# Performance work log

Hardware: AMD Instinct MI355X
Metric: run time of the kernel (lower is better)

The kernel has to match this reference:

```python
import jax, jax.numpy as jnp
import numpy as np

N_NODES = 100000
N_EDGES = 3200000
HIDDEN = 64
OUT = 30


def _graph_conv(x, src, dst, W, b, n_nodes):
    # DGL GraphConv with norm='both': D_out^{-1/2} -> aggregate -> D_in^{-1/2} -> W -> +b
    ones = jnp.ones(src.shape[0], dtype=x.dtype)
    deg_out = jax.ops.segment_sum(ones, src, num_segments=n_nodes)
    deg_in = jax.ops.segment_sum(ones, dst, num_segments=n_nodes)
    norm_out = jnp.where(deg_out > 0, jax.lax.rsqrt(jnp.maximum(deg_out, 1e-30)), 0.0)
    norm_in = jnp.where(deg_in > 0, jax.lax.rsqrt(jnp.maximum(deg_in, 1e-30)), 0.0)
    h = x * norm_out[:, None]                    # [N, F] scaled source features
    msg = h[src]                                 # [E, F] gather
    agg = jax.ops.segment_sum(msg, dst, num_segments=n_nodes)  # [N, F] scatter-add
    agg = agg * norm_in[:, None]
    return agg @ W + b


def setup_inputs() -> dict:
    key = jax.random.key(0)
    k1, k2, k3, k4, k5 = jax.random.split(key, 5)
    x = jax.random.normal(k1, (N_NODES, HIDDEN), dtype=jnp.float32)
    src = jax.random.randint(k2, (N_EDGES,), 0, N_NODES, dtype=jnp.int32)
    dst = jax.random.randint(k3, (N_EDGES,), 0, N_NODES, dtype=jnp.int32)
    W1 = jax.random.normal(k4, (HIDDEN, HIDDEN), dtype=jnp.float32) / np.sqrt(HIDDEN)
    b1 = jnp.zeros((HIDDEN,), dtype=jnp.float32)
    W2 = jax.random.normal(k5, (HIDDEN, OUT), dtype=jnp.float32) / np.sqrt(HIDDEN)
    b2 = jnp.zeros((OUT,), dtype=jnp.float32)
    return {"x": x, "src": src, "dst": dst, "W1": W1, "b1": b1, "W2": W2, "b2": b2}


def reference(x, src, dst, W1, b1, W2, b2):
    h = _graph_conv(x, src, dst, W1, b1, N_NODES)
    h = jax.nn.relu(h)                           # conv1 activation=F.relu
    out = _graph_conv(h, src, dst, W2, b2, N_NODES)  # conv2: no activation
    return out
```

## Files before the change

kernel.cpp:

```cpp
#include <hip/hip_runtime.h>


#define NN 100000
#define NE 3200000
#define NOUTF 30
#define TPB 256
#define TPBW 1024
#define TPBS 512

#define DSH 8
#define DCB 256
#define DNB ((NN + DCB - 1) / DCB)
#define SSH 10
#define SCB 1024
#define SNB ((NN + SCB - 1) / SCB)

#define CHUNK 8192
#define NBLK ((NE + CHUNK - 1) / CHUNK)
#define HLD (DNB * NBLK)
#define HLS (SNB * NBLK)
#define HLT (HLD + HLS)
#define EPT (CHUNK / TPBS)

#define GCH 1024
#define NSC ((HLT + GCH - 1) / GCH)

#define POOL 9216

__device__ __forceinline__ unsigned short f2bf(float f) {
  unsigned u = __float_as_uint(f);
  u = (u + 0x7FFFu + ((u >> 16) & 1u)) >> 16;
  return (unsigned short)u;
}

__device__ __forceinline__ void acc8(float* a, const uint4& u) {
  a[0] += __uint_as_float(u.x << 16);
  a[1] += __uint_as_float(u.x & 0xFFFF0000u);
  a[2] += __uint_as_float(u.y << 16);
  a[3] += __uint_as_float(u.y & 0xFFFF0000u);
  a[4] += __uint_as_float(u.z << 16);
  a[5] += __uint_as_float(u.z & 0xFFFF0000u);
  a[6] += __uint_as_float(u.w << 16);
  a[7] += __uint_as_float(u.w & 0xFFFF0000u);
}

__device__ __forceinline__ int xcd_swz(int orig, int n) {
  int q = n / 8, r = n % 8;
  int xcd = orig % 8, idx = orig / 8;
  return (xcd < r ? xcd * (q + 1) : r * (q + 1) + (xcd - r) * q) + idx;
}

__global__ __launch_bounds__(TPBW) void k_hist(const int* __restrict__ src,
                                               const int* __restrict__ dst,
                                               int* __restrict__ H) {
  __shared__ int hd[DNB], hs[SNB];
  int t = threadIdx.x, k = blockIdx.x;
  for (int b = t; b < DNB; b += TPBW) hd[b] = 0;
  for (int b = t; b < SNB; b += TPBW) hs[b] = 0;
  __syncthreads();
  int beg = k * CHUNK, end = min(NE, beg + CHUNK);
  for (int i = beg + t; i < end; i += TPBW) {
    atomicAdd(&hd[dst[i] >> DSH], 1);
    atomicAdd(&hs[src[i] >> SSH], 1);
  }
  __syncthreads();
  for (int b = t; b < DNB; b += TPBW) H[b * NBLK + k] = hd[b];
  for (int b = t; b < SNB; b += TPBW) H[HLD + b * NBLK + k] = hs[b];
}

__global__ __launch_bounds__(TPB) void g_scan1(const int* __restrict__ a,
                                               int* __restrict__ bsums) {
  int t = threadIdx.x;
  int base = blockIdx.x * GCH + t * 4;
  int s = 0;
#pragma unroll
  for (int j = 0; j < 4; ++j) { int idx = base + j; if (idx < HLT) s += a[idx]; }
  __shared__ int red[TPB];
  red[t] = s; __syncthreads();
  for (int off = TPB / 2; off > 0; off >>= 1) {
    if (t < off) red[t] += red[t + off];
    __syncthreads();
  }
  if (t == 0) bsums[blockIdx.x] = red[0];
}

__global__ __launch_bounds__(1024) void g_scan2(int* __restrict__ bsums) {
  int t = threadIdx.x;
  __shared__ int lds[1024];
  int v = (t < NSC) ? bsums[t] : 0;
  int acc = v; lds[t] = acc; __syncthreads();
  for (int off = 1; off < 1024; off <<= 1) {
    int add = (t >= off) ? lds[t - off] : 0; __syncthreads();
    acc += add; lds[t] = acc; __syncthreads();
  }
  if (t < NSC) bsums[t] = acc - v;
}

__global__ __launch_bounds__(TPB) void g_scan3(int* __restrict__ a,
                                               const int* __restrict__ bsums) {
  int t = threadIdx.x;
  int base = blockIdx.x * GCH + t * 4;
  int v[4]; int s = 0;
#pragma unroll
  for (int j = 0; j < 4; ++j) {
    int idx = base + j;
    v[j] = (idx < HLT) ? a[idx] : 0;
    s += v[j];
  }
  __shared__ int lds[TPB];
  int acc = s; lds[t] = acc; __syncthreads();
  for (int off = 1; off < TPB; off <<= 1) {
    int add = (t >= off) ? lds[t - off] : 0; __syncthreads();
    acc += add; lds[t] = acc; __syncthreads();
  }
  int run = bsums[blockIdx.x] + (acc - s);
#pragma unroll
  for (int j = 0; j < 4; ++j) {
    int idx = base + j;
    if (idx < HLT) a[idx] = run;
    run += v[j];
  }
}

__global__ __launch_bounds__(TPBS) void k_scatter(const int* __restrict__ src,
                                                  const int* __restrict__ dst,
                                                  const int* __restrict__ Hsc,
                                                  int* __restrict__ packed,
                                                  unsigned short* __restrict__ ss) {
  __shared__ int pack_lds[CHUNK];
  __shared__ unsigned short ss_lds[CHUNK];
  __shared__ int baseD[DNB + 1], curD[DNB];
  __shared__ int baseS[SNB + 1], curS[SNB];
  __shared__ int scanbuf[TPBS];
  int t = threadIdx.x;
  int k = xcd_swz((int)blockIdx.x, NBLK);
  int beg = k * CHUNK, end = min(NE, beg + CHUNK);
  int cnt = end - beg;

  int es[EPT], ed[EPT];
#pragma unroll
  for (int j = 0; j < EPT; ++j) {
    int i = beg + j * TPBS + t;
    if (i < end) { es[j] = src[i]; ed[j] = dst[i]; }
    else { es[j] = -1; ed[j] = -1; }
  }

  for (int b = t; b < DNB; b += TPBS) curD[b] = 0;
  for (int b = t; b < SNB; b += TPBS) curS[b] = 0;
  __syncthreads();
#pragma unroll
  for (int j = 0; j < EPT; ++j) {
    if (ed[j] >= 0) {
      atomicAdd(&curD[ed[j] >> DSH], 1);
      atomicAdd(&curS[es[j] >> SSH], 1);
    }
  }
  __syncthreads();

  {
    int v = (t < DNB) ? curD[t] : 0;
    int acc = v; scanbuf[t] = acc; __syncthreads();
    for (int off = 1; off < TPBS; off <<= 1) {
      int add = (t >= off) ? scanbuf[t - off] : 0; __syncthreads();
      acc += add; scanbuf[t] = acc; __syncthreads();
    }
    if (t < DNB) baseD[t] = acc - v;
    if (t == 0) baseD[DNB] = cnt;
  }
  __syncthreads();
  {
    int v = (t < SNB) ? curS[t] : 0;
    int acc = v; scanbuf[t] = acc; __syncthreads();
    for (int off = 1; off < TPBS; off <<= 1) {
      int add = (t >= off) ? scanbuf[t - off] : 0; __syncthreads();
      acc += add; scanbuf[t] = acc; __syncthreads();
    }
    if (t < SNB) baseS[t] = acc - v;
    if (t == 0) baseS[SNB] = cnt;
  }
  __syncthreads();
  for (int b = t; b < DNB; b += TPBS) curD[b] = baseD[b];
  for (int b = t; b < SNB; b += TPBS) curS[b] = baseS[b];
  __syncthreads();

#pragma unroll
  for (int j = 0; j < EPT; ++j) {
    if (ed[j] >= 0) {
      int p = atomicAdd(&curD[ed[j] >> DSH], 1);
      pack_lds[p] = (es[j] << DSH) | (ed[j] & (DCB - 1));
      int q = atomicAdd(&curS[es[j] >> SSH], 1);
      ss_lds[q] = (unsigned short)(es[j] & (SCB - 1));
    }
  }
  __syncthreads();

  for (int i = t; i < cnt; i += TPBS) {
    int lo = 0, hi = DNB;
    while (hi - lo > 1) { int mid = (lo + hi) >> 1; if (baseD[mid] <= i) lo = mid; else hi = mid; }
    packed[Hsc[lo * NBLK + k] + (i - baseD[lo])] = pack_lds[i];
  }
  for (int i = t; i < cnt; i += TPBS) {
    int lo = 0, hi = SNB;
    while (hi - lo > 1) { int mid = (lo + hi) >> 1; if (baseS[mid] <= i) lo = mid; else hi = mid; }
    ss[Hsc[HLD + lo * NBLK + k] + (i - baseS[lo]) - NE] = ss_lds[i];
  }
}

__global__ __launch_bounds__(TPB) void k_fine_sort(const int* __restrict__ Hsc,
                                                   const int* __restrict__ packed,
                                                   int* __restrict__ src_sorted,
                                                   int* __restrict__ row_ptr,
                                                   float* __restrict__ norm_in) {
  __shared__ int hist[DCB], scn[DCB], cur[DCB];
  __shared__ int pool[POOL];
  int t = threadIdx.x, b = blockIdx.x;
  int seg_beg = Hsc[b * NBLK];
  int seg_end = (b + 1 < DNB) ? Hsc[(b + 1) * NBLK] : NE;
  int cnt = seg_end - seg_beg;
  hist[t] = 0;
  __syncthreads();
  for (int i = seg_beg + t; i < seg_end; i += TPB)
    atomicAdd(&hist[packed[i] & (DCB - 1)], 1);
  __syncthreads();
  scn[t] = hist[t];
  __syncthreads();
  for (int off = 1; off < DCB; off <<= 1) {
    int add = (t >= off) ? scn[t - off] : 0;
    __syncthreads();
    scn[t] += add;
    __syncthreads();
  }
  {
    int excl = scn[t] - hist[t];
    cur[t] = excl;
    int node = b * DCB + t;
    if (node < NN) {
      row_ptr[node] = seg_beg + excl;
      norm_in[node] = (hist[t] > 0) ? rsqrtf((float)hist[t]) : 0.0f;
    }
  }
  if (b == DNB - 1 && t == 0) row_ptr[NN] = NE;
  __syncthreads();
  for (int i = seg_beg + t; i < seg_end; i += TPB) {
    int v = packed[i];
    int p = atomicAdd(&cur[v & (DCB - 1)], 1);
    int sv = v >> DSH;
    if (p < POOL) pool[p] = sv;
    else src_sorted[seg_beg + p] = sv;
  }
  __syncthreads();
  int lim = min(cnt, POOL);
  for (int i = t; i < lim; i += TPB) src_sorted[seg_beg + i] = pool[i];
}

__global__ __launch_bounds__(TPB) void k_fine_count(const int* __restrict__ Hsc,
                                                    const unsigned short* __restrict__ ss,
                                                    float* __restrict__ norm_out) {
  __shared__ int hist[SCB];
  int t = threadIdx.x, b = blockIdx.x;
  int seg_beg = Hsc[HLD + b * NBLK] - NE;
  int seg_end = (b + 1 < SNB) ? Hsc[HLD + (b + 1) * NBLK] - NE : NE;
  for (int i = t; i < SCB; i += TPB) hist[i] = 0;
  __syncthreads();
  for (int i = seg_beg + t; i < seg_end; i += TPB)
    atomicAdd(&hist[ss[i]], 1);
  __syncthreads();
  for (int i = t; i < SCB; i += TPB) {
    int node = b * SCB + i;
    if (node < NN)
      norm_out[node] = (hist[i] > 0) ? rsqrtf((float)hist[i]) : 0.0f;
  }
}

__global__ __launch_bounds__(TPB) void k_gemm1(const float4* __restrict__ x4,
                                               const float* __restrict__ W1,
                                               const float* __restrict__ norm_out,
                                               unsigned short* __restrict__ xt_b) {
  int lane = threadIdx.x & 63;
  int wid = (blockIdx.x * TPB + threadIdx.x) >> 6;
  int nwaves = gridDim.x * (TPB / 64);
  float w[64];
#pragma unroll
  for (int k = 0; k < 64; ++k) w[k] = W1[k * 64 + lane];
  int m = lane >> 4, q = lane & 15;
  for (int grp = wid; grp < NN / 4; grp += nwaves) {
    int nbase = grp * 4;
    float4 rv = x4[(nbase + m) * 16 + q];
    int r0 = __float_as_int(rv.x), r1 = __float_as_int(rv.y);
    int r2 = __float_as_int(rv.z), r3 = __float_as_int(rv.w);
    float acc[4] = {0.f, 0.f, 0.f, 0.f};
#pragma unroll
    for (int mm = 0; mm < 4; ++mm) {
#pragma unroll
      for (int ql = 0; ql < 16; ++ql) {
        int sl = mm * 16 + ql;
        acc[mm] = fmaf(__int_as_float(__builtin_amdgcn_readlane(r0, sl)), w[ql * 4 + 0], acc[mm]);
        acc[mm] = fmaf(__int_as_float(__builtin_amdgcn_readlane(r1, sl)), w[ql * 4 + 1], acc[mm]);
        acc[mm] = fmaf(__int_as_float(__builtin_amdgcn_readlane(r2, sl)), w[ql * 4 + 2], acc[mm]);
        acc[mm] = fmaf(__int_as_float(__builtin_amdgcn_readlane(r3, sl)), w[ql * 4 + 3], acc[mm]);
      }
    }
#pragma unroll
    for (int mm = 0; mm < 4; ++mm) {
      int n = nbase + mm;
      xt_b[n * 64 + lane] = f2bf(norm_out[n] * acc[mm]);
    }
  }
}

__global__ __launch_bounds__(TPB) void k_agg1(const uint4* __restrict__ xt4,
                                              const int* __restrict__ src_sorted,
                                              const int* __restrict__ row_ptr,
                                              const float* __restrict__ norm_in,
                                              const float* __restrict__ b1,
                                              uint4* __restrict__ h1_b4) {
  int node = (blockIdx.x * TPB + threadIdx.x) >> 6;
  int lane = threadIdx.x & 63;
  int slot = lane >> 3;
  int fl = lane & 7;
  int beg = row_ptr[node];
  int end = row_ptr[node + 1];
  float a[8] = {0.f, 0.f, 0.f, 0.f, 0.f, 0.f, 0.f, 0.f};
  int e = beg + slot;
  for (; e + 8 < end; e += 16) {
    int s0 = src_sorted[e];
    int s1 = src_sorted[e + 8];
    uint4 u0 = xt4[s0 * 8 + fl];
    uint4 u1 = xt4[s1 * 8 + fl];
    acc8(a, u0);
    acc8(a, u1);
  }
  if (e < end) {
    uint4 u0 = xt4[src_sorted[e] * 8 + fl];
    acc8(a, u0);
  }
#pragma unroll
  for (int off = 8; off <= 32; off <<= 1) {
#pragma unroll
    for (int j = 0; j < 8; ++j) a[j] += __shfl_xor(a[j], off);
  }
  if (slot == 0) {
    float ni = norm_in[node];
    const float4* b1_4 = reinterpret_cast<const float4*>(b1);
    float4 bl = b1_4[fl * 2];
    float4 bh = b1_4[fl * 2 + 1];
    float v0 = fmaxf(fmaf(a[0], ni, bl.x), 0.f);
    float v1 = fmaxf(fmaf(a[1], ni, bl.y), 0.f);
    float v2 = fmaxf(fmaf(a[2], ni, bl.z), 0.f);
    float v3 = fmaxf(fmaf(a[3], ni, bl.w), 0.f);
    float v4 = fmaxf(fmaf(a[4], ni, bh.x), 0.f);
    float v5 = fmaxf(fmaf(a[5], ni, bh.y), 0.f);
    float v6 = fmaxf(fmaf(a[6], ni, bh.z), 0.f);
    float v7 = fmaxf(fmaf(a[7], ni, bh.w), 0.f);
    uint4 o;
    o.x = (unsigned)f2bf(v0) | ((unsigned)f2bf(v1) << 16);
    o.y = (unsigned)f2bf(v2) | ((unsigned)f2bf(v3) << 16);
    o.z = (unsigned)f2bf(v4) | ((unsigned)f2bf(v5) << 16);
    o.w = (unsigned)f2bf(v6) | ((unsigned)f2bf(v7) << 16);
    h1_b4[node * 8 + fl] = o;
  }
}

__global__ __launch_bounds__(TPB) void k_gemm2b(const uint4* __restrict__ h1b4,
                                                const float* __restrict__ W2,
                                                const float* __restrict__ norm_out,
                                                unsigned short* __restrict__ h1t_b) {
  int lane = threadIdx.x & 63;
  int wid = (blockIdx.x * TPB + threadIdx.x) >> 6;
  int nwaves = gridDim.x * (TPB / 64);
  int oc = lane & 31;
  float w[64];
#pragma unroll
  for (int k = 0; k < 64; ++k)
    w[k] = (oc < NOUTF) ? W2[k * NOUTF + oc] : 0.f;
  int r = lane >> 3, q = lane & 7;
  for (int grp = wid; grp < NN / 8; grp += nwaves) {
    int nbase = grp * 8;
    uint4 rv = h1b4[(nbase + r) * 8 + q];
    int v0 = (int)rv.x, v1 = (int)rv.y, v2 = (int)rv.z, v3 = (int)rv.w;
#pragma unroll
    for (int rr = 0; rr < 8; ++rr) {
      float acc0 = 0.f, acc1 = 0.f;
#pragma unroll
      for (int qq = 0; qq < 8; ++qq) {
        int sl = rr * 8 + qq;
        unsigned u0 = (unsigned)__builtin_amdgcn_readlane(v0, sl);
        unsigned u1 = (unsigned)__builtin_amdgcn_readlane(v1, sl);
        unsigned u2 = (unsigned)__builtin_amdgcn_readlane(v2, sl);
        unsigned u3 = (unsigned)__builtin_amdgcn_readlane(v3, sl);
        acc0 = fmaf(__uint_as_float(u0 << 16),          w[qq * 8 + 0], acc0);
        acc1 = fmaf(__uint_as_float(u0 & 0xFFFF0000u), w[qq * 8 + 1], acc1);
        acc0 = fmaf(__uint_as_float(u1 << 16),          w[qq * 8 + 2], acc0);
        acc1 = fmaf(__uint_as_float(u1 & 0xFFFF0000u), w[qq * 8 + 3], acc1);
        acc0 = fmaf(__uint_as_float(u2 << 16),          w[qq * 8 + 4], acc0);
        acc1 = fmaf(__uint_as_float(u2 & 0xFFFF0000u), w[qq * 8 + 5], acc1);
        acc0 = fmaf(__uint_as_float(u3 << 16),          w[qq * 8 + 6], acc0);
        acc1 = fmaf(__uint_as_float(u3 & 0xFFFF0000u), w[qq * 8 + 7], acc1);
      }
      int n = nbase + rr;
      if (lane < 32) {
        float acc = acc0 + acc1;
        unsigned short hv = (oc < NOUTF) ? f2bf(norm_out[n] * acc) : (unsigned short)0;
        h1t_b[n * 32 + oc] = hv;
      }
    }
  }
}

__global__ __launch_bounds__(TPB) void k_agg2(const uint4* __restrict__ h1t4,
                                              const int* __restrict__ src_sorted,
                                              const int* __restrict__ row_ptr,
                                              const float* __restrict__ norm_in,
                                              const float* __restrict__ b2,
                                              float* __restrict__ out) {
  int node = (blockIdx.x * TPB + threadIdx.x) >> 6;
  int lane = threadIdx.x & 63;
  int slot = lane >> 2;
  int fl = lane & 3;
  int beg = row_ptr[node];
  int end = row_ptr[node + 1];
  float a[8] = {0.f, 0.f, 0.f, 0.f, 0.f, 0.f, 0.f, 0.f};
  int e = beg + slot;
  for (; e + 16 < end; e += 32) {
    int s0 = src_sorted[e];
    int s1 = src_sorted[e + 16];
    uint4 u0 = h1t4[s0 * 4 + fl];
    uint4 u1 = h1t4[s1 * 4 + fl];
    acc8(a, u0);
    acc8(a, u1);
  }
  if (e < end) {
    uint4 u0 = h1t4[src_sorted[e] * 4 + fl];
    acc8(a, u0);
  }
#pragma unroll
  for (int off = 4; off <= 32; off <<= 1) {
#pragma unroll
    for (int j = 0; j < 8; ++j) a[j] += __shfl_xor(a[j], off);
  }
  if (slot == 0) {
    float ni = norm_in[node];
    int f0 = fl * 8;
    float2* ob = (float2*)(out + (size_t)node * NOUTF);
#pragma unroll
    for (int p = 0; p < 4; ++p) {
      int f = f0 + p * 2;
      if (f < NOUTF) {
        float2 v;
        v.x = fmaf(a[p * 2], ni, b2[f]);
        v.y = fmaf(a[p * 2 + 1], ni, b2[f + 1]);
        ob[f >> 1] = v;
      }
    }
  }
}

extern "C" void kernel_launch(void* const* d_in, const int* in_sizes, int n_in,
                              void* d_out, int out_size, void* d_ws, size_t ws_size,
                              hipStream_t stream) {
  (void)in_sizes; (void)n_in; (void)out_size; (void)ws_size;
  const float* x = (const float*)d_in[0];
  const int* src = (const int*)d_in[1];
  const int* dst = (const int*)d_in[2];
  const float* W1 = (const float*)d_in[3];
  const float* b1 = (const float*)d_in[4];
  const float* W2 = (const float*)d_in[5];
  const float* b2 = (const float*)d_in[6];
  float* out = (float*)d_out;

  char* ws = (char*)d_ws;
  int* row_ptr = (int*)(ws + 0);
  float* norm_out = (float*)(ws + 400128);
  float* norm_in = (float*)(ws + 800128);
  int* H = (int*)(ws + 1200128);
  int* bsums = (int*)(ws + 1964928);
  unsigned short* ss = (unsigned short*)(ws + 1965696);
  int* src_sorted = (int*)(ws + 8365696);
  int* packed = (int*)(ws + 21165696);
  uint4* h1_b4 = (uint4*)(ws + 21165696);
  unsigned short* xt_b = (unsigned short*)(ws + 46765696);
  unsigned short* h1t_b = (unsigned short*)(ws + 46765696);

  k_hist<<<NBLK, TPBW, 0, stream>>>(src, dst, H);
  g_scan1<<<NSC, TPB, 0, stream>>>(H, bsums);
  g_scan2<<<1, 1024, 0, stream>>>(bsums);
  g_scan3<<<NSC, TPB, 0, stream>>>(H, bsums);
  k_scatter<<<NBLK, TPBS, 0, stream>>>(src, dst, H, packed, ss);
  k_fine_sort<<<DNB, TPB, 0, stream>>>(H, packed, src_sorted, row_ptr, norm_in);
  k_fine_count<<<SNB, TPB, 0, stream>>>(H, ss, norm_out);
  k_gemm1<<<1024, TPB, 0, stream>>>((const float4*)x, W1, norm_out, xt_b);
  k_agg1<<<NN / 4, TPB, 0, stream>>>((const uint4*)xt_b, src_sorted, row_ptr,
                                     norm_in, b1, h1_b4);
  k_gemm2b<<<1024, TPB, 0, stream>>>((const uint4*)h1_b4, W2, norm_out, h1t_b);
  k_agg2<<<NN / 4, TPB, 0, stream>>>((const uint4*)h1t_b, src_sorted, row_ptr, norm_in, b2, out);
}
```

Baseline: 269.9 us.

## Shrink radix bucket widths and pack source keys into bytes

Halves the destination bucket width (256→128 nodes) and quarters the source bucket width (1024→256), doubling and quadrupling the number of coarse buckets. The source-key array drops from 16-bit to 8-bit. The in-block scan is adapted to two elements per thread, and the workspace offsets are moved. The aim is more fine-sort blocks with smaller LDS pools, which should give better occupancy and less key traffic. In exchange the histogram and scan arrays grow, along with the scatter's per-block bucket count and its binary-search depth.

```diff
diff --git a/kernel.cpp b/kernel.cpp
--- a/kernel.cpp
+++ b/kernel.cpp
@@ -8,11 +8,11 @@
 #define TPBW 1024
 #define TPBS 512
 
-#define DSH 8
-#define DCB 256
+#define DSH 7
+#define DCB 128
 #define DNB ((NN + DCB - 1) / DCB)
-#define SSH 10
-#define SCB 1024
+#define SSH 8
+#define SCB 256
 #define SNB ((NN + SCB - 1) / SCB)
 
 #define CHUNK 8192
@@ -25,7 +25,7 @@
 #define GCH 1024
 #define NSC ((HLT + GCH - 1) / GCH)
 
-#define POOL 9216
+#define POOL 4608
 
 __device__ __forceinline__ unsigned short f2bf(float f) {
   unsigned u = __float_as_uint(f);
@@ -126,9 +126,9 @@
                                                   const int* __restrict__ dst,
                                                   const int* __restrict__ Hsc,
                                                   int* __restrict__ packed,
-                                                  unsigned short* __restrict__ ss) {
+                                                  unsigned char* __restrict__ ss) {
   __shared__ int pack_lds[CHUNK];
-  __shared__ unsigned short ss_lds[CHUNK];
+  __shared__ unsigned char ss_lds[CHUNK];
   __shared__ int baseD[DNB + 1], curD[DNB];
   __shared__ int baseS[SNB + 1], curS[SNB];
   __shared__ int scanbuf[TPBS];
@@ -158,13 +158,18 @@
   __syncthreads();
 
   {
-    int v = (t < DNB) ? curD[t] : 0;
-    int acc = v; scanbuf[t] = acc; __syncthreads();
+    int i0 = t * 2, i1 = t * 2 + 1;
+    int v0 = (i0 < DNB) ? curD[i0] : 0;
+    int v1 = (i1 < DNB) ? curD[i1] : 0;
+    int s = v0 + v1;
+    int acc = s; scanbuf[t] = acc; __syncthreads();
     for (int off = 1; off < TPBS; off <<= 1) {
       int add = (t >= off) ? scanbuf[t - off] : 0; __syncthreads();
       acc += add; scanbuf[t] = acc; __syncthreads();
     }
-    if (t < DNB) baseD[t] = acc - v;
+    int excl = acc - s;
+    if (i0 < DNB) baseD[i0] = excl;
+    if (i1 < DNB) baseD[i1] = excl + v0;
     if (t == 0) baseD[DNB] = cnt;
   }
   __syncthreads();
@@ -189,7 +194,7 @@
       int p = atomicAdd(&curD[ed[j] >> DSH], 1);
       pack_lds[p] = (es[j] << DSH) | (ed[j] & (DCB - 1));
       int q = atomicAdd(&curS[es[j] >> SSH], 1);
-      ss_lds[q] = (unsigned short)(es[j] & (SCB - 1));
+      ss_lds[q] = (unsigned char)(es[j] & (SCB - 1));
     }
   }
   __syncthreads();
@@ -217,20 +222,20 @@
   int seg_beg = Hsc[b * NBLK];
   int seg_end = (b + 1 < DNB) ? Hsc[(b + 1) * NBLK] : NE;
   int cnt = seg_end - seg_beg;
-  hist[t] = 0;
+  if (t < DCB) hist[t] = 0;
   __syncthreads();
   for (int i = seg_beg + t; i < seg_end; i += TPB)
     atomicAdd(&hist[packed[i] & (DCB - 1)], 1);
   __syncthreads();
-  scn[t] = hist[t];
+  if (t < DCB) scn[t] = hist[t];
   __syncthreads();
   for (int off = 1; off < DCB; off <<= 1) {
-    int add = (t >= off) ? scn[t - off] : 0;
+    int add = (t >= off && t < DCB) ? scn[t - off] : 0;
     __syncthreads();
-    scn[t] += add;
+    if (t < DCB) scn[t] += add;
     __syncthreads();
   }
-  {
+  if (t < DCB) {
     int excl = scn[t] - hist[t];
     cur[t] = excl;
     int node = b * DCB + t;
@@ -254,21 +259,21 @@
 }
 
 __global__ __launch_bounds__(TPB) void k_fine_count(const int* __restrict__ Hsc,
-                                                    const unsigned short* __restrict__ ss,
+                                                    const unsigned char* __restrict__ ss,
                                                     float* __restrict__ norm_out) {
   __shared__ int hist[SCB];
   int t = threadIdx.x, b = blockIdx.x;
   int seg_beg = Hsc[HLD + b * NBLK] - NE;
   int seg_end = (b + 1 < SNB) ? Hsc[HLD + (b + 1) * NBLK] - NE : NE;
-  for (int i = t; i < SCB; i += TPB) hist[i] = 0;
+  if (t < SCB) hist[t] = 0;
   __syncthreads();
   for (int i = seg_beg + t; i < seg_end; i += TPB)
     atomicAdd(&hist[ss[i]], 1);
   __syncthreads();
-  for (int i = t; i < SCB; i += TPB) {
-    int node = b * SCB + i;
+  if (t < SCB) {
+    int node = b * SCB + t;
     if (node < NN)
-      norm_out[node] = (hist[i] > 0) ? rsqrtf((float)hist[i]) : 0.0f;
+      norm_out[node] = (hist[t] > 0) ? rsqrtf((float)hist[t]) : 0.0f;
   }
 }
 
@@ -473,8 +478,8 @@
   float* norm_out = (float*)(ws + 400128);
   float* norm_in = (float*)(ws + 800128);
   int* H = (int*)(ws + 1200128);
-  int* bsums = (int*)(ws + 1964928);
-  unsigned short* ss = (unsigned short*)(ws + 1965696);
+  int* bsums = (int*)(ws + 3100128);
+  unsigned char* ss = (unsigned char*)(ws + 3101952);
   int* src_sorted = (int*)(ws + 8365696);
   int* packed = (int*)(ws + 21165696);
   uint4* h1_b4 = (uint4*)(ws + 21165696);
```

New measurement: 248.8 us. -7.8%, faster.
